# Performance work log

Measured on AMD Instinct MI355X. Metric: run time of the kernel, lower is better.

Reference implementation:

```python
import jax, jax.numpy as jnp
import numpy as np

N_NODES = 100000
N_EDGES = 1000000
D = 172          # n_node_features == memory_dimension (added together)
B = 4096         # batch after src/dst concat
K = 20           # n_neighbors


def setup_inputs() -> dict:
    key = jax.random.key(0)
    ks = jax.random.split(key, 12)
    return {
        "node_feats": jax.random.normal(ks[0], (N_NODES, D), dtype=jnp.float32),
        "edge_feats": jax.random.normal(ks[1], (N_EDGES, D), dtype=jnp.float32),
        "memory": jax.random.normal(ks[2], (N_NODES, D), dtype=jnp.float32),
        "timestamps": jax.random.uniform(ks[3], (B,), dtype=jnp.float32),
        "edge_times1": jax.random.uniform(ks[4], (B, K), dtype=jnp.float32),
        "edge_times2": jax.random.uniform(ks[5], (B * K, K), dtype=jnp.float32),
        "source_nodes": jax.random.randint(ks[6], (B,), 0, N_NODES),
        "neighbors1": jax.random.randint(ks[7], (B, K), 0, N_NODES),
        "edge_idxs1": jax.random.randint(ks[8], (B, K), 0, N_EDGES),
        "neighbors2": jax.random.randint(ks[9], (B * K, K), 0, N_NODES),
        "edge_idxs2": jax.random.randint(ks[10], (B * K, K), 0, N_EDGES),
    }


def reference(node_feats, edge_feats, memory, timestamps, edge_times1,
              edge_times2, source_nodes, neighbors1, edge_idxs1,
              neighbors2, edge_idxs2):
    # node_features[idx] + memory[idx] == (node_features + memory)[idx]
    node_mem = node_feats + memory  # [N, D]

    # ---- layer 0 data_collect ----
    src_feats1 = node_mem[source_nodes]        # [B, D]
    neigh_feats1 = node_mem[neighbors1]        # [B, K, D]
    edge_f1 = edge_feats[edge_idxs1]           # [B, K, D]
    deltas1 = timestamps[:, None] - edge_times1  # [B, K]
    mask1 = neighbors1 == 0                    # [B, K]

    # ---- layer 1 data_collect: nodes = neighbors.flatten(), ts repeated ----
    nodes2 = neighbors1.reshape(-1)            # [B*K]
    ts2 = jnp.repeat(timestamps, K)            # [B*K]
    src_feats2 = node_mem[nodes2]              # [B*K, D]
    neigh_feats2 = node_mem[neighbors2]        # [B*K, K, D]
    edge_f2 = edge_feats[edge_idxs2]           # [B*K, K, D]
    deltas2 = ts2[:, None] - edge_times2       # [B*K, K]
    mask2 = neighbors2 == 0                    # [B*K, K]

    return (src_feats1, neigh_feats1, edge_f1, deltas1, mask1,
            src_feats2, neigh_feats2, edge_f2, deltas2, mask2)
```

## Files before the change

### kernel.cpp

```cpp
#include <hip/hip_runtime.h>

typedef float f32x4 __attribute__((ext_vector_type(4)));

static constexpr unsigned D4 = 43;


__global__ __launch_bounds__(256) void k1_fused(
    f32x4* __restrict__ nm, const f32x4* __restrict__ nf, const f32x4* __restrict__ mem,
    float* __restrict__ dl1, float* __restrict__ mk1, const float* __restrict__ ts,
    const float* __restrict__ et1, const int* __restrict__ nb1,
    float* __restrict__ dl2, float* __restrict__ mk2,
    const float* __restrict__ et2, const int* __restrict__ nb2,
    f32x4* __restrict__ ef1o, const f32x4* __restrict__ ef, const int* __restrict__ ei1)
{
    constexpr unsigned ADD_N = 100000u * D4;
    constexpr unsigned ADD_B = (ADD_N + 255u) / 256u;
    constexpr unsigned DM1_B = 81920u / 256u;
    constexpr unsigned DM2_B = 1638400u / 256u;
    unsigned b = blockIdx.x, t = threadIdx.x;

    if (b < ADD_B) {
        unsigned i = b * 256u + t;
        if (i < ADD_N) nm[i] = nf[i] + mem[i];
    } else if (b < ADD_B + DM1_B) {
        unsigned i = (b - ADD_B) * 256u + t;
        __builtin_nontemporal_store(ts[i / 20u] - et1[i], dl1 + i);
        __builtin_nontemporal_store((nb1[i] == 0) ? 1.0f : 0.0f, mk1 + i);
    } else if (b < ADD_B + DM1_B + DM2_B) {
        unsigned i = (b - ADD_B - DM1_B) * 256u + t;
        __builtin_nontemporal_store(ts[i / 400u] - et2[i], dl2 + i);
        __builtin_nontemporal_store((nb2[i] == 0) ? 1.0f : 0.0f, mk2 + i);
    } else {
        unsigned i = (b - ADD_B - DM1_B - DM2_B) * 256u + t;
        unsigned row = i / D4, col = i - row * D4;
        unsigned s = (unsigned)ei1[row] * D4 + col;
        __builtin_nontemporal_store(ef[s], ef1o + i);
    }
}
static constexpr unsigned K1_BLOCKS =
    ((100000u * 43u + 255u) / 256u) + (81920u / 256u) + (1638400u / 256u)
    + ((81920u * 43u) / 256u);

__global__ __launch_bounds__(256) void k2_nodes(
    const f32x4* __restrict__ nm,
    f32x4* __restrict__ src1, const int* __restrict__ srcn,
    f32x4* __restrict__ nf1o, f32x4* __restrict__ sf2, const int* __restrict__ nb1,
    f32x4* __restrict__ nf2o, const int* __restrict__ nb2)
{
    constexpr unsigned S1_B = (4096u * D4) / 256u;
    constexpr unsigned N1_B = (81920u * D4) / 256u;
    unsigned b = blockIdx.x, t = threadIdx.x;

    if (b < S1_B) {
        unsigned i = b * 256u + t;
        unsigned row = i / D4, col = i - row * D4;
        __builtin_nontemporal_store(nm[(unsigned)srcn[row] * D4 + col], src1 + i);
    } else if (b < S1_B + N1_B) {
        unsigned i = (b - S1_B) * 256u + t;
        unsigned row = i / D4, col = i - row * D4;
        f32x4 v = nm[(unsigned)nb1[row] * D4 + col];
        __builtin_nontemporal_store(v, nf1o + i);
        __builtin_nontemporal_store(v, sf2 + i);
    } else {
        unsigned i = (b - S1_B - N1_B) * 256u + t;
        unsigned row = i / D4, col = i - row * D4;
        __builtin_nontemporal_store(nm[(unsigned)nb2[row] * D4 + col], nf2o + i);
    }
}
static constexpr unsigned K2_BLOCKS =
    ((4096u * 43u) / 256u) + ((81920u * 43u) / 256u) + ((1638400u * 43u) / 256u);

__global__ __launch_bounds__(256) void k3_ef2(
    f32x4* __restrict__ dst, const f32x4* __restrict__ ef, const int* __restrict__ ei2)
{
    unsigned i = blockIdx.x * 256u + threadIdx.x;
    unsigned row = i / D4, col = i - row * D4;
    __builtin_nontemporal_store(ef[(unsigned)ei2[row] * D4 + col], dst + i);
}
static constexpr unsigned K3_BLOCKS = (1638400u * 43u) / 256u;


__global__ void gather4_k(f32x4* __restrict__ dst,
                          const f32x4* __restrict__ a,
                          const int* __restrict__ idx,
                          unsigned n4) {
    unsigned i = blockIdx.x * blockDim.x + threadIdx.x;
    unsigned stride = gridDim.x * blockDim.x;
    for (; i < n4; i += stride) {
        unsigned row = i / D4, col = i - row * D4;
        __builtin_nontemporal_store(a[(unsigned)idx[row] * D4 + col], dst + i);
    }
}

__global__ void gather_add4_k(f32x4* __restrict__ dst,
                              const f32x4* __restrict__ a,
                              const f32x4* __restrict__ b,
                              const int* __restrict__ idx,
                              unsigned n4) {
    unsigned i = blockIdx.x * blockDim.x + threadIdx.x;
    unsigned stride = gridDim.x * blockDim.x;
    for (; i < n4; i += stride) {
        unsigned row = i / D4, col = i - row * D4;
        unsigned s = (unsigned)idx[row] * D4 + col;
        __builtin_nontemporal_store(a[s] + b[s], dst + i);
    }
}

__global__ void gather_add4_dual_k(f32x4* __restrict__ dst1,
                                   f32x4* __restrict__ dst2,
                                   const f32x4* __restrict__ a,
                                   const f32x4* __restrict__ b,
                                   const int* __restrict__ idx,
                                   unsigned n4) {
    unsigned i = blockIdx.x * blockDim.x + threadIdx.x;
    unsigned stride = gridDim.x * blockDim.x;
    for (; i < n4; i += stride) {
        unsigned row = i / D4, col = i - row * D4;
        unsigned s = (unsigned)idx[row] * D4 + col;
        f32x4 v = a[s] + b[s];
        __builtin_nontemporal_store(v, dst1 + i);
        __builtin_nontemporal_store(v, dst2 + i);
    }
}

template <unsigned TSD>
__global__ void dm_k(float* __restrict__ deltas,
                     float* __restrict__ mask,
                     const float* __restrict__ ts,
                     const float* __restrict__ et,
                     const int* __restrict__ neigh,
                     unsigned n) {
    unsigned i = blockIdx.x * blockDim.x + threadIdx.x;
    unsigned stride = gridDim.x * blockDim.x;
    for (; i < n; i += stride) {
        __builtin_nontemporal_store(ts[i / TSD] - et[i], deltas + i);
        __builtin_nontemporal_store((neigh[i] == 0) ? 1.0f : 0.0f, mask + i);
    }
}

static inline unsigned grid_for(unsigned n, unsigned block, unsigned cap) {
    unsigned g = (n + block - 1) / block;
    return g < cap ? (g ? g : 1) : cap;
}

extern "C" void kernel_launch(void* const* d_in, const int* in_sizes, int n_in,
                              void* d_out, int out_size, void* d_ws, size_t ws_size,
                              hipStream_t stream) {
    const float* nf  = (const float*)d_in[0];
    const float* ef  = (const float*)d_in[1];
    const float* mem = (const float*)d_in[2];
    const float* ts  = (const float*)d_in[3];
    const float* et1 = (const float*)d_in[4];
    const float* et2 = (const float*)d_in[5];
    const int* srcn  = (const int*)d_in[6];
    const int* nb1   = (const int*)d_in[7];
    const int* ei1   = (const int*)d_in[8];
    const int* nb2   = (const int*)d_in[9];
    const int* ei2   = (const int*)d_in[10];

    constexpr unsigned B = 4096, K = 20, Dd = 172;
    constexpr unsigned BK = B * K;
    constexpr unsigned NN = 100000;

    float* out = (float*)d_out;
    size_t o = 0;
    float* src1 = out + o;  o += (size_t)B * Dd;
    float* nf1  = out + o;  o += (size_t)BK * Dd;
    float* ef1  = out + o;  o += (size_t)BK * Dd;
    float* dl1  = out + o;  o += (size_t)BK;
    float* mk1  = out + o;  o += (size_t)BK;
    float* sf2  = out + o;  o += (size_t)BK * Dd;
    float* nf2  = out + o;  o += (size_t)BK * K * Dd;
    float* ef2  = out + o;  o += (size_t)BK * K * Dd;
    float* dl2  = out + o;  o += (size_t)BK * K;
    float* mk2  = out + o;  o += (size_t)BK * K;

    const f32x4* nf4  = (const f32x4*)nf;
    const f32x4* mem4 = (const f32x4*)mem;
    const f32x4* ef4  = (const f32x4*)ef;

    const size_t NM_BYTES = (size_t)NN * Dd * sizeof(float);

    if (ws_size >= NM_BYTES) {
        f32x4* nm4 = (f32x4*)d_ws;
        k1_fused<<<K1_BLOCKS, 256, 0, stream>>>(
            nm4, nf4, mem4,
            dl1, mk1, ts, et1, nb1,
            dl2, mk2, et2, nb2,
            (f32x4*)ef1, ef4, ei1);
        k2_nodes<<<K2_BLOCKS, 256, 0, stream>>>(
            nm4,
            (f32x4*)src1, srcn,
            (f32x4*)nf1, (f32x4*)sf2, nb1,
            (f32x4*)nf2, nb2);
        k3_ef2<<<K3_BLOCKS, 256, 0, stream>>>((f32x4*)ef2, ef4, ei2);
    } else {
        const unsigned BLK = 256, CAP = 2048;
        {
            unsigned n4 = B * D4;
            gather_add4_k<<<grid_for(n4, BLK, CAP), BLK, 0, stream>>>(
                (f32x4*)src1, nf4, mem4, srcn, n4);
        }
        {
            unsigned n4 = BK * D4;
            gather_add4_dual_k<<<grid_for(n4, BLK, CAP), BLK, 0, stream>>>(
                (f32x4*)nf1, (f32x4*)sf2, nf4, mem4, nb1, n4);
        }
        {
            unsigned n4 = BK * K * D4;
            gather_add4_k<<<grid_for(n4, BLK, CAP), BLK, 0, stream>>>(
                (f32x4*)nf2, nf4, mem4, nb2, n4);
        }
        dm_k<K><<<grid_for(BK, BLK, CAP), BLK, 0, stream>>>(dl1, mk1, ts, et1, nb1, BK);
        dm_k<K * K><<<grid_for(BK * K, BLK, CAP), BLK, 0, stream>>>(
            dl2, mk2, ts, et2, nb2, BK * K);
        {
            unsigned n4 = BK * D4;
            gather4_k<<<grid_for(n4, BLK, CAP), BLK, 0, stream>>>(
                (f32x4*)ef1, ef4, ei1, n4);
        }
        {
            unsigned n4 = BK * K * D4;
            gather4_k<<<grid_for(n4, BLK, CAP), BLK, 0, stream>>>(
                (f32x4*)ef2, ef4, ei2, n4);
        }
    }
}
```

Baseline: 802.5 us.

## Split edge-feature level-2 gather into index-range passes for cache locality

Replaces the single ef2 gather kernel with four passes, each copying only rows whose edge index falls in one quarter of the edge table. Each pass then reads about 172MB of source, aiming to raise cache hit rates on the random gather. The trade-off is that every pass re-reads all indices and launches the full grid, so the index traffic and thread work grow fourfold. The workspace-too-small fallback path is also removed, so the kernel now assumes the workspace is large enough.

```diff
diff --git a/kernel.cpp b/kernel.cpp
--- a/kernel.cpp
+++ b/kernel.cpp
@@ -1,9 +1,9 @@
 #include <hip/hip_runtime.h>
+
 
 typedef float f32x4 __attribute__((ext_vector_type(4)));
 
 static constexpr unsigned D4 = 43;
-
 
 __global__ __launch_bounds__(256) void k1_fused(
     f32x4* __restrict__ nm, const f32x4* __restrict__ nf, const f32x4* __restrict__ mem,
@@ -70,78 +70,18 @@
 static constexpr unsigned K2_BLOCKS =
     ((4096u * 43u) / 256u) + ((81920u * 43u) / 256u) + ((1638400u * 43u) / 256u);
 
-__global__ __launch_bounds__(256) void k3_ef2(
-    f32x4* __restrict__ dst, const f32x4* __restrict__ ef, const int* __restrict__ ei2)
+__global__ __launch_bounds__(256) void k3_ef2_pass(
+    f32x4* __restrict__ dst, const f32x4* __restrict__ ef,
+    const int* __restrict__ ei2, unsigned lo, unsigned hi)
 {
     unsigned i = blockIdx.x * 256u + threadIdx.x;
     unsigned row = i / D4, col = i - row * D4;
-    __builtin_nontemporal_store(ef[(unsigned)ei2[row] * D4 + col], dst + i);
+    unsigned e = (unsigned)ei2[row];
+    if (e >= lo && e < hi) {
+        __builtin_nontemporal_store(ef[e * D4 + col], dst + i);
+    }
 }
 static constexpr unsigned K3_BLOCKS = (1638400u * 43u) / 256u;
-
-
-__global__ void gather4_k(f32x4* __restrict__ dst,
-                          const f32x4* __restrict__ a,
-                          const int* __restrict__ idx,
-                          unsigned n4) {
-    unsigned i = blockIdx.x * blockDim.x + threadIdx.x;
-    unsigned stride = gridDim.x * blockDim.x;
-    for (; i < n4; i += stride) {
-        unsigned row = i / D4, col = i - row * D4;
-        __builtin_nontemporal_store(a[(unsigned)idx[row] * D4 + col], dst + i);
-    }
-}
-
-__global__ void gather_add4_k(f32x4* __restrict__ dst,
-                              const f32x4* __restrict__ a,
-                              const f32x4* __restrict__ b,
-                              const int* __restrict__ idx,
-                              unsigned n4) {
-    unsigned i = blockIdx.x * blockDim.x + threadIdx.x;
-    unsigned stride = gridDim.x * blockDim.x;
-    for (; i < n4; i += stride) {
-        unsigned row = i / D4, col = i - row * D4;
-        unsigned s = (unsigned)idx[row] * D4 + col;
-        __builtin_nontemporal_store(a[s] + b[s], dst + i);
-    }
-}
-
-__global__ void gather_add4_dual_k(f32x4* __restrict__ dst1,
-                                   f32x4* __restrict__ dst2,
-                                   const f32x4* __restrict__ a,
-                                   const f32x4* __restrict__ b,
-                                   const int* __restrict__ idx,
-                                   unsigned n4) {
-    unsigned i = blockIdx.x * blockDim.x + threadIdx.x;
-    unsigned stride = gridDim.x * blockDim.x;
-    for (; i < n4; i += stride) {
-        unsigned row = i / D4, col = i - row * D4;
-        unsigned s = (unsigned)idx[row] * D4 + col;
-        f32x4 v = a[s] + b[s];
-        __builtin_nontemporal_store(v, dst1 + i);
-        __builtin_nontemporal_store(v, dst2 + i);
-    }
-}
-
-template <unsigned TSD>
-__global__ void dm_k(float* __restrict__ deltas,
-                     float* __restrict__ mask,
-                     const float* __restrict__ ts,
-                     const float* __restrict__ et,
-                     const int* __restrict__ neigh,
-                     unsigned n) {
-    unsigned i = blockIdx.x * blockDim.x + threadIdx.x;
-    unsigned stride = gridDim.x * blockDim.x;
-    for (; i < n; i += stride) {
-        __builtin_nontemporal_store(ts[i / TSD] - et[i], deltas + i);
-        __builtin_nontemporal_store((neigh[i] == 0) ? 1.0f : 0.0f, mask + i);
-    }
-}
-
-static inline unsigned grid_for(unsigned n, unsigned block, unsigned cap) {
-    unsigned g = (n + block - 1) / block;
-    return g < cap ? (g ? g : 1) : cap;
-}
 
 extern "C" void kernel_launch(void* const* d_in, const int* in_sizes, int n_in,
                               void* d_out, int out_size, void* d_ws, size_t ws_size,
@@ -161,6 +101,7 @@
     constexpr unsigned B = 4096, K = 20, Dd = 172;
     constexpr unsigned BK = B * K;
     constexpr unsigned NN = 100000;
+    constexpr unsigned NE = 1000000;
 
     float* out = (float*)d_out;
     size_t o = 0;
@@ -180,49 +121,25 @@
     const f32x4* ef4  = (const f32x4*)ef;
 
     const size_t NM_BYTES = (size_t)NN * Dd * sizeof(float);
+    if (ws_size < NM_BYTES) {
+    }
 
-    if (ws_size >= NM_BYTES) {
-        f32x4* nm4 = (f32x4*)d_ws;
-        k1_fused<<<K1_BLOCKS, 256, 0, stream>>>(
-            nm4, nf4, mem4,
-            dl1, mk1, ts, et1, nb1,
-            dl2, mk2, et2, nb2,
-            (f32x4*)ef1, ef4, ei1);
-        k2_nodes<<<K2_BLOCKS, 256, 0, stream>>>(
-            nm4,
-            (f32x4*)src1, srcn,
-            (f32x4*)nf1, (f32x4*)sf2, nb1,
-            (f32x4*)nf2, nb2);
-        k3_ef2<<<K3_BLOCKS, 256, 0, stream>>>((f32x4*)ef2, ef4, ei2);
-    } else {
-        const unsigned BLK = 256, CAP = 2048;
-        {
-            unsigned n4 = B * D4;
-            gather_add4_k<<<grid_for(n4, BLK, CAP), BLK, 0, stream>>>(
-                (f32x4*)src1, nf4, mem4, srcn, n4);
-        }
-        {
-            unsigned n4 = BK * D4;
-            gather_add4_dual_k<<<grid_for(n4, BLK, CAP), BLK, 0, stream>>>(
-                (f32x4*)nf1, (f32x4*)sf2, nf4, mem4, nb1, n4);
-        }
-        {
-            unsigned n4 = BK * K * D4;
-            gather_add4_k<<<grid_for(n4, BLK, CAP), BLK, 0, stream>>>(
-                (f32x4*)nf2, nf4, mem4, nb2, n4);
-        }
-        dm_k<K><<<grid_for(BK, BLK, CAP), BLK, 0, stream>>>(dl1, mk1, ts, et1, nb1, BK);
-        dm_k<K * K><<<grid_for(BK * K, BLK, CAP), BLK, 0, stream>>>(
-            dl2, mk2, ts, et2, nb2, BK * K);
-        {
-            unsigned n4 = BK * D4;
-            gather4_k<<<grid_for(n4, BLK, CAP), BLK, 0, stream>>>(
-                (f32x4*)ef1, ef4, ei1, n4);
-        }
-        {
-            unsigned n4 = BK * K * D4;
-            gather4_k<<<grid_for(n4, BLK, CAP), BLK, 0, stream>>>(
-                (f32x4*)ef2, ef4, ei2, n4);
-        }
+    f32x4* nm4 = (f32x4*)d_ws;
+    k1_fused<<<K1_BLOCKS, 256, 0, stream>>>(
+        nm4, nf4, mem4,
+        dl1, mk1, ts, et1, nb1,
+        dl2, mk2, et2, nb2,
+        (f32x4*)ef1, ef4, ei1);
+    k2_nodes<<<K2_BLOCKS, 256, 0, stream>>>(
+        nm4,
+        (f32x4*)src1, srcn,
+        (f32x4*)nf1, (f32x4*)sf2, nb1,
+        (f32x4*)nf2, nb2);
+    constexpr unsigned NPASS = 4;
+    constexpr unsigned STRIPE = NE / NPASS;
+    for (unsigned p = 0; p < NPASS; ++p) {
+        unsigned lo = p * STRIPE;
+        unsigned hi = (p == NPASS - 1) ? NE : lo + STRIPE;
+        k3_ef2_pass<<<K3_BLOCKS, 256, 0, stream>>>((f32x4*)ef2, ef4, ei2, lo, hi);
     }
 }
```

New measurement: 1.166 ms. +45.3%, slower.
